# Kernel tuning notes

Hardware: AMD Instinct MI355X
Metric: run time of the kernel (lower is better)

## Reference

```python
import jax, jax.numpy as jnp
import numpy as np

NUM_FEAT = 10
C_IN = 64


def setup_inputs() -> dict:
    key = jax.random.key(0)
    ks = jax.random.split(key, 8)
    B, T, C, H, W = 1, 8, C_IN, 32, 32
    scale = 1.0 / np.sqrt(C)
    return {
        "input1": jax.random.normal(ks[0], (B, T, C, H, W), dtype=jnp.float32),
        "input2": jax.random.normal(ks[1], (B, T, C, H, W), dtype=jnp.float32),
        "w1": jax.random.normal(ks[2], (NUM_FEAT, C), dtype=jnp.float32) * scale,
        "b1": jax.random.normal(ks[3], (NUM_FEAT,), dtype=jnp.float32) * scale,
        "w2": jax.random.normal(ks[4], (NUM_FEAT, C), dtype=jnp.float32) * scale,
        "b2": jax.random.normal(ks[5], (NUM_FEAT,), dtype=jnp.float32) * scale,
        "w3": jax.random.normal(ks[6], (NUM_FEAT, C), dtype=jnp.float32) * scale,
        "b3": jax.random.normal(ks[7], (NUM_FEAT,), dtype=jnp.float32) * scale,
    }


def reference(input1, input2, w1, b1, w2, b2, w3, b3):
    B, T, C, H, W = input1.shape
    N = T * H * W
    # transpose(1,2).reshape -> [B, C, T*H*W]
    x1 = input1.transpose(0, 2, 1, 3, 4).reshape(B, C, N)
    x2 = input2.transpose(0, 2, 1, 3, 4).reshape(B, C, N)
    # 1x1 Conv1d projections (act == 0 -> ReLU branch)
    q = jnp.einsum('fc,bcn->bnf', w1, x1) + b1            # [B, N, F]
    k = jnp.einsum('fc,bcn->bfn', w2, x2) + b2[:, None]   # [B, F, N]
    v = jnp.einsum('fc,bcn->bnf', w3, x1) + b3            # [B, N, F]
    scores = jax.nn.relu(jnp.einsum('bnf,bfm->bnm', q, k))  # [B, N, N]
    out = jnp.einsum('bnm,bmf->bnf', scores, v)             # [B, N, F]
    # view([B,T,H,W,F]).permute(0,1,4,2,3)
    return out.reshape(B, T, H, W, -1).transpose(0, 1, 4, 2, 3)
```

## Files before the change

kernel.cpp:

```cpp
#include <hip/hip_runtime.h>

typedef short  s4  __attribute__((ext_vector_type(4)));
typedef float  f4  __attribute__((ext_vector_type(4)));
typedef unsigned int u2v __attribute__((ext_vector_type(2)));
typedef unsigned int uint32;
typedef unsigned short ushort16;

#define NF     10
#define CIN    64
#define NTOT   8192
#define HW     1024
#define FPAD   16
#define MSPLIT 8
#define MCHUNK (NTOT / MSPLIT)

#if defined(__has_builtin) && __has_builtin(__builtin_amdgcn_mfma_f32_16x16x16bf16_1k)
#define MFMA16(a, b, c) __builtin_amdgcn_mfma_f32_16x16x16bf16_1k((a), (b), (c), 0, 0, 0)
#else
static __device__ inline f4 mfma16_asm(s4 a, s4 b, f4 c) {
    f4 d;
    asm volatile("s_nop 1\n\t"
                 "v_mfma_f32_16x16x16_bf16 %0, %1, %2, %3\n\t"
                 "s_nop 7\n\ts_nop 7"
                 : "=v"(d) : "v"(a), "v"(b), "v"(c));
    return d;
}
#define MFMA16(a, b, c) mfma16_asm((a), (b), (c))
#endif

static __device__ inline ushort16 f32_to_bf16_rne(float x) {
    uint32 u = __builtin_bit_cast(uint32, x);
    u = (u + 0x7fffu + ((u >> 16) & 1u)) >> 16;
    return (ushort16)u;
}

__global__ __launch_bounds__(256) void qkv_bf16_kernel(
    const float* __restrict__ in1, const float* __restrict__ in2,
    const float* __restrict__ w1, const float* __restrict__ b1,
    const float* __restrict__ w2, const float* __restrict__ b2,
    const float* __restrict__ w3, const float* __restrict__ b3,
    ushort16* __restrict__ qb, ushort16* __restrict__ kb,
    ushort16* __restrict__ vT)
{
    const int which = blockIdx.y;
    const float* x = (which == 1) ? in2 : in1;
    const float* w = (which == 0) ? w1 : ((which == 1) ? w2 : w3);
    const float* b = (which == 0) ? b1 : ((which == 1) ? b2 : b3);

    const int n  = blockIdx.x * 256 + threadIdx.x;
    const int t  = n >> 10;
    const int hw = n & 1023;
    const float* p = x + (size_t)t * (CIN * HW) + hw;

    float acc[NF];
#pragma unroll
    for (int f = 0; f < NF; ++f) acc[f] = b[f];
#pragma unroll 8
    for (int c = 0; c < CIN; ++c) {
        float a = p[c * HW];
#pragma unroll
        for (int f = 0; f < NF; ++f) acc[f] = fmaf(w[f * CIN + c], a, acc[f]);
    }

    if (which == 2) {
#pragma unroll
        for (int f = 0; f < NF; ++f) vT[(size_t)f * NTOT + n] = f32_to_bf16_rne(acc[f]);
    } else {
        ushort16 row[FPAD];
#pragma unroll
        for (int f = 0; f < NF; ++f) row[f] = f32_to_bf16_rne(acc[f]);
#pragma unroll
        for (int f = NF; f < FPAD; ++f) row[f] = 0;
        ushort16* dst = ((which == 0) ? qb : kb) + (size_t)n * FPAD;
        ((uint4*)dst)[0] = ((const uint4*)row)[0];
        ((uint4*)dst)[1] = ((const uint4*)row)[1];
    }
}

__global__ __launch_bounds__(256) void attn_mfma_kernel(
    const ushort16* __restrict__ qb, const ushort16* __restrict__ kb,
    const ushort16* __restrict__ vT, float* __restrict__ out)
{
    const int lane = threadIdx.x & 63;
    const int wid  = threadIdx.x >> 6;
    const int row  = lane & 15;
    const int quad = lane >> 4;
    const int n0   = blockIdx.x * 64 + wid * 16;
    const int m0   = blockIdx.y * MCHUNK;

    const s4 qf = *(const s4*)(qb + (size_t)(n0 + row) * FPAD + 4 * quad);

    const s4* kp = (const s4*)(kb + (size_t)(m0 + row) * FPAD + 4 * quad);
    const s4* vp = (const s4*)(vT + (size_t)row * NTOT + m0 + 4 * quad);

    f4 acc  = {0.f, 0.f, 0.f, 0.f};
    const f4 zero = {0.f, 0.f, 0.f, 0.f};

#pragma unroll 8
    for (int s = 0; s < MCHUNK / 16; ++s) {
        s4 kf = kp[s * 64];
        s4 vf = vp[s * 4];

        f4 sc = MFMA16(kf, qf, zero);

        float r0 = fmaxf(sc[0], 0.f), r1 = fmaxf(sc[1], 0.f);
        float r2 = fmaxf(sc[2], 0.f), r3 = fmaxf(sc[3], 0.f);
        uint32 lo = __builtin_amdgcn_perm(__builtin_bit_cast(uint32, r1),
                                          __builtin_bit_cast(uint32, r0), 0x07060302u);
        uint32 hi = __builtin_amdgcn_perm(__builtin_bit_cast(uint32, r3),
                                          __builtin_bit_cast(uint32, r2), 0x07060302u);
        s4 pb = __builtin_bit_cast(s4, (u2v){lo, hi});

        acc = MFMA16(vf, pb, acc);
    }

    const int n  = n0 + row;
    const int t  = n >> 10;
    const int hw = n & 1023;
    float* op = out + (size_t)t * (NF * HW) + hw;
    const int fbase = 4 * quad;
#pragma unroll
    for (int r = 0; r < 4; ++r) {
        int f = fbase + r;
        if (f < NF) atomicAdd(op + f * HW, acc[r]);
    }
}

extern "C" void kernel_launch(void* const* d_in, const int* in_sizes, int n_in,
                              void* d_out, int out_size, void* d_ws, size_t ws_size,
                              hipStream_t stream)
{
    const float* in1 = (const float*)d_in[0];
    const float* in2 = (const float*)d_in[1];
    const float* w1  = (const float*)d_in[2];
    const float* b1  = (const float*)d_in[3];
    const float* w2  = (const float*)d_in[4];
    const float* b2  = (const float*)d_in[5];
    const float* w3  = (const float*)d_in[6];
    const float* b3  = (const float*)d_in[7];

    ushort16* qb = (ushort16*)d_ws;
    ushort16* kb = qb + (size_t)NTOT * FPAD;
    ushort16* vT = kb + (size_t)NTOT * FPAD;
    float* out = (float*)d_out;

    hipMemsetAsync(d_out, 0, (size_t)out_size * sizeof(float), stream);

    qkv_bf16_kernel<<<dim3(NTOT / 256, 3), 256, 0, stream>>>(
        in1, in2, w1, b1, w2, b2, w3, b3, qb, kb, vT);

    attn_mfma_kernel<<<dim3(NTOT / 64, MSPLIT), 256, 0, stream>>>(qb, kb, vT, out);
}
```

Measured before the change: 115.0 us.

## Tile V for coalesced MFMA loads, fuse Q/V projection, replace atomics with reduce

The projection kernel now computes Q and V together from one read of input1 and writes V in an MFMA-fragment tile layout. The attention kernel can then load each V fragment with one contiguous per-lane load instead of strided row reads. The per-split atomicAdd into the output and the memset are replaced by plain partial-sum stores to a workspace, followed by a separate reduction kernel that also does the final layout. This adds one kernel launch and extra workspace traffic, and the projection blocks shrink to 64 threads.

```diff
diff --git a/kernel.cpp b/kernel.cpp
--- a/kernel.cpp
+++ b/kernel.cpp
@@ -6,13 +6,14 @@
 typedef unsigned int uint32;
 typedef unsigned short ushort16;
 
-#define NF     10
-#define CIN    64
-#define NTOT   8192
-#define HW     1024
-#define FPAD   16
-#define MSPLIT 8
-#define MCHUNK (NTOT / MSPLIT)
+#define NF      10
+#define CIN     64
+#define NTOT    8192
+#define HW      1024
+#define FPAD    16
+#define MSPLIT  8
+#define MCHUNK  (NTOT / MSPLIT)
+#define PSTRIDE 16
 
 #if defined(__has_builtin) && __has_builtin(__builtin_amdgcn_mfma_f32_16x16x16bf16_1k)
 #define MFMA16(a, b, c) __builtin_amdgcn_mfma_f32_16x16x16bf16_1k((a), (b), (c), 0, 0, 0)
@@ -34,52 +35,71 @@
     return (ushort16)u;
 }
 
-__global__ __launch_bounds__(256) void qkv_bf16_kernel(
+__global__ __launch_bounds__(64) void qkv_kernel(
     const float* __restrict__ in1, const float* __restrict__ in2,
     const float* __restrict__ w1, const float* __restrict__ b1,
     const float* __restrict__ w2, const float* __restrict__ b2,
     const float* __restrict__ w3, const float* __restrict__ b3,
     ushort16* __restrict__ qb, ushort16* __restrict__ kb,
-    ushort16* __restrict__ vT)
+    ushort16* __restrict__ vtile)
 {
-    const int which = blockIdx.y;
-    const float* x = (which == 1) ? in2 : in1;
-    const float* w = (which == 0) ? w1 : ((which == 1) ? w2 : w3);
-    const float* b = (which == 0) ? b1 : ((which == 1) ? b2 : b3);
-
-    const int n  = blockIdx.x * 256 + threadIdx.x;
+    const int n  = blockIdx.x * 64 + threadIdx.x;
     const int t  = n >> 10;
     const int hw = n & 1023;
-    const float* p = x + (size_t)t * (CIN * HW) + hw;
 
-    float acc[NF];
+    if (blockIdx.y == 0) {
+        const float* p = in1 + (size_t)t * (CIN * HW) + hw;
+        float aq[NF], av[NF];
 #pragma unroll
-    for (int f = 0; f < NF; ++f) acc[f] = b[f];
+        for (int f = 0; f < NF; ++f) { aq[f] = b1[f]; av[f] = b3[f]; }
 #pragma unroll 8
-    for (int c = 0; c < CIN; ++c) {
-        float a = p[c * HW];
+        for (int c = 0; c < CIN; ++c) {
+            float a = p[c * HW];
 #pragma unroll
-        for (int f = 0; f < NF; ++f) acc[f] = fmaf(w[f * CIN + c], a, acc[f]);
-    }
-
-    if (which == 2) {
-#pragma unroll
-        for (int f = 0; f < NF; ++f) vT[(size_t)f * NTOT + n] = f32_to_bf16_rne(acc[f]);
-    } else {
+            for (int f = 0; f < NF; ++f) {
+                aq[f] = fmaf(w1[f * CIN + c], a, aq[f]);
+                av[f] = fmaf(w3[f * CIN + c], a, av[f]);
+            }
+        }
         ushort16 row[FPAD];
 #pragma unroll
-        for (int f = 0; f < NF; ++f) row[f] = f32_to_bf16_rne(acc[f]);
+        for (int f = 0; f < NF; ++f) row[f] = f32_to_bf16_rne(aq[f]);
 #pragma unroll
         for (int f = NF; f < FPAD; ++f) row[f] = 0;
-        ushort16* dst = ((which == 0) ? qb : kb) + (size_t)n * FPAD;
-        ((uint4*)dst)[0] = ((const uint4*)row)[0];
-        ((uint4*)dst)[1] = ((const uint4*)row)[1];
+        ushort16* dq = qb + (size_t)n * FPAD;
+        ((uint4*)dq)[0] = ((const uint4*)row)[0];
+        ((uint4*)dq)[1] = ((const uint4*)row)[1];
+        const int tile = n >> 4, mi = n & 15;
+        const int quad = mi >> 2, jj = mi & 3;
+        ushort16* vb = vtile + (size_t)tile * 256 + jj;
+#pragma unroll
+        for (int f = 0; f < FPAD; ++f)
+            vb[(quad * 16 + f) * 4] = (f < NF) ? f32_to_bf16_rne(av[f]) : (ushort16)0;
+    } else {
+        const float* p = in2 + (size_t)t * (CIN * HW) + hw;
+        float ak[NF];
+#pragma unroll
+        for (int f = 0; f < NF; ++f) ak[f] = b2[f];
+#pragma unroll 8
+        for (int c = 0; c < CIN; ++c) {
+            float a = p[c * HW];
+#pragma unroll
+            for (int f = 0; f < NF; ++f) ak[f] = fmaf(w2[f * CIN + c], a, ak[f]);
+        }
+        ushort16 row[FPAD];
+#pragma unroll
+        for (int f = 0; f < NF; ++f) row[f] = f32_to_bf16_rne(ak[f]);
+#pragma unroll
+        for (int f = NF; f < FPAD; ++f) row[f] = 0;
+        ushort16* dk = kb + (size_t)n * FPAD;
+        ((uint4*)dk)[0] = ((const uint4*)row)[0];
+        ((uint4*)dk)[1] = ((const uint4*)row)[1];
     }
 }
 
 __global__ __launch_bounds__(256) void attn_mfma_kernel(
     const ushort16* __restrict__ qb, const ushort16* __restrict__ kb,
-    const ushort16* __restrict__ vT, float* __restrict__ out)
+    const ushort16* __restrict__ vtile, float* __restrict__ pws)
 {
     const int lane = threadIdx.x & 63;
     const int wid  = threadIdx.x >> 6;
@@ -89,17 +109,16 @@
     const int m0   = blockIdx.y * MCHUNK;
 
     const s4 qf = *(const s4*)(qb + (size_t)(n0 + row) * FPAD + 4 * quad);
+    const s4* kp = (const s4*)(kb + (size_t)(m0 + row) * FPAD + 4 * quad);
+    const s4* vp = (const s4*)(vtile + (size_t)(m0 >> 4) * 256) + lane;
 
-    const s4* kp = (const s4*)(kb + (size_t)(m0 + row) * FPAD + 4 * quad);
-    const s4* vp = (const s4*)(vT + (size_t)row * NTOT + m0 + 4 * quad);
-
-    f4 acc  = {0.f, 0.f, 0.f, 0.f};
+    f4 acc = {0.f, 0.f, 0.f, 0.f};
     const f4 zero = {0.f, 0.f, 0.f, 0.f};
 
 #pragma unroll 8
     for (int s = 0; s < MCHUNK / 16; ++s) {
         s4 kf = kp[s * 64];
-        s4 vf = vp[s * 4];
+        s4 vf = vp[s * 64];
 
         f4 sc = MFMA16(kf, qf, zero);
 
@@ -114,16 +133,28 @@
         acc = MFMA16(vf, pb, acc);
     }
 
-    const int n  = n0 + row;
-    const int t  = n >> 10;
-    const int hw = n & 1023;
-    float* op = out + (size_t)t * (NF * HW) + hw;
+    const int n = n0 + row;
     const int fbase = 4 * quad;
 #pragma unroll
     for (int r = 0; r < 4; ++r) {
         int f = fbase + r;
-        if (f < NF) atomicAdd(op + f * HW, acc[r]);
+        if (f < NF)
+            pws[((size_t)blockIdx.y * PSTRIDE + f) * NTOT + n] = acc[r];
     }
+}
+
+__global__ __launch_bounds__(256) void reduce_kernel(
+    const float* __restrict__ pws, float* __restrict__ out)
+{
+    const int gid = blockIdx.x * 256 + threadIdx.x;
+    const int f = gid >> 13;
+    const int n = gid & (NTOT - 1);
+    float s = 0.f;
+#pragma unroll
+    for (int y = 0; y < MSPLIT; ++y)
+        s += pws[((size_t)y * PSTRIDE + f) * NTOT + n];
+    const int t = n >> 10, hw = n & 1023;
+    out[(size_t)t * (NF * HW) + f * HW + hw] = s;
 }
 
 extern "C" void kernel_launch(void* const* d_in, const int* in_sizes, int n_in,
@@ -139,15 +170,16 @@
     const float* w3  = (const float*)d_in[6];
     const float* b3  = (const float*)d_in[7];
 
-    ushort16* qb = (ushort16*)d_ws;
-    ushort16* kb = qb + (size_t)NTOT * FPAD;
-    ushort16* vT = kb + (size_t)NTOT * FPAD;
-    float* out = (float*)d_out;
+    ushort16* qb    = (ushort16*)d_ws;
+    ushort16* kb    = qb + (size_t)NTOT * FPAD;
+    ushort16* vtile = kb + (size_t)NTOT * FPAD;
+    float*    pws   = (float*)(vtile + (size_t)NTOT * FPAD);
+    float*    out   = (float*)d_out;
 
-    hipMemsetAsync(d_out, 0, (size_t)out_size * sizeof(float), stream);
+    qkv_kernel<<<dim3(NTOT / 64, 2), 64, 0, stream>>>(
+        in1, in2, w1, b1, w2, b2, w3, b3, qb, kb, vtile);
 
-    qkv_bf16_kernel<<<dim3(NTOT / 256, 3), 256, 0, stream>>>(
-        in1, in2, w1, b1, w2, b2, w3, b3, qb, kb, vT);
+    attn_mfma_kernel<<<dim3(NTOT / 64, MSPLIT), 256, 0, stream>>>(qb, kb, vtile, pws);
 
-    attn_mfma_kernel<<<dim3(NTOT / 64, MSPLIT), 256, 0, stream>>>(qb, kb, vT, out);
+    reduce_kernel<<<dim3(NF * NTOT / 256), 256, 0, stream>>>(pws, out);
 }
```

Measured after the change: 110.2 us. 1.04x faster.
